# Kernel optimization log

Measured on AMD Instinct MI355X. Metric: run time of the kernel, lower is better.

## Reference

```python
import jax, jax.numpy as jnp
import numpy as np

B, S, ENC2, DEC = 32, 4096, 1024, 512

def setup_inputs() -> dict:
    key = jax.random.key(0)
    k1, k2, k3 = jax.random.split(key, 3)
    hidden = jax.random.normal(k1, (B, DEC), dtype=jnp.float32)
    context = jax.random.normal(k2, (B, S, ENC2), dtype=jnp.float32)
    mask = jnp.ones((B, S), dtype=jnp.int32)
    # Linear(enc*2+dec -> dec): weight [DEC, ENC2+DEC], bias [DEC]
    W_attn = jax.random.normal(k3, (DEC, ENC2 + DEC), dtype=jnp.float32) * (1.0 / np.sqrt(ENC2 + DEC))
    b_attn = jnp.zeros((DEC,), dtype=jnp.float32)
    v = jax.random.uniform(jax.random.fold_in(key, 7), (DEC,), dtype=jnp.float32)
    return {"hidden": hidden, "context": context, "mask": mask,
            "W_attn": W_attn, "b_attn": b_attn, "v": v}

def reference(hidden, context, mask, W_attn, b_attn, v):
    # cat((hidden repeated over S, context)) @ W.T == hidden@Wh.T + context@Wc.T
    # split W to avoid materializing the [B,S,1536] concat
    Wh = W_attn[:, :DEC]          # acts on hidden (first in cat)
    Wc = W_attn[:, DEC:]          # acts on context
    h_proj = hidden @ Wh.T + b_attn                      # [B, DEC]
    c_proj = jnp.einsum('bse,de->bsd', context, Wc)      # [B, S, DEC]
    sim = jnp.tanh(h_proj[:, None, :] + c_proj)          # [B, S, DEC]
    scores = jnp.einsum('bsd,d->bs', sim, v)             # [B, S]
    scores = jnp.where(mask == 0, -jnp.inf, scores)
    return jax.nn.softmax(scores, axis=1)
```

## Files before the change

kernel.cpp:

```cpp
#include <hip/hip_runtime.h>
#include <hip/hip_bf16.h>
#include <cmath>

#define NB 32
#define NS 4096
#define NK 1024
#define ND 512
#define WSTRIDE 1536
#define NTO 16

using bf16x8 = __attribute__((ext_vector_type(8))) __bf16;
using u16x8  = __attribute__((ext_vector_type(8))) unsigned short;
using f32x4  = __attribute__((ext_vector_type(4))) float;
typedef unsigned short u16;

__device__ inline u16 f2b(float x) {
    __hip_bfloat16 h = __float2bfloat16(x);
    u16 u; __builtin_memcpy(&u, &h, 2); return u;
}

__device__ inline float fast_tanh(float x) {
    float xc = fminf(fmaxf(x, -10.f), 10.f);
    float e = __expf(2.f * xc);
    return (e - 1.f) / (e + 1.f);
}

__global__ void pack_wc_kernel(const float* __restrict__ W, u16* __restrict__ wcb) {
    int idx = blockIdx.x * 256 + threadIdx.x;
    int R = idx >> 10, k = idx & 1023;
    float val = W[(size_t)R * WSTRIDE + ND + k];
    int ks = k >> 5, S = (k >> 3) & 3, j = k & 7;
    int g = ((R << 2) + S) ^ (R & 7);
    wcb[(ks << 14) + (g << 3) + j] = f2b(val);
}

__global__ void hproj_kernel(const float* __restrict__ hidden, const float* __restrict__ W,
                             const float* __restrict__ bias, float* __restrict__ hp) {
    int b = blockIdx.x, d = threadIdx.x;
    __shared__ float sh[ND];
    sh[d] = hidden[b * ND + d];
    __syncthreads();
    const float4* wr = (const float4*)(W + (size_t)d * WSTRIDE);
    float acc = bias[d];
#pragma unroll 8
    for (int k = 0; k < ND / 4; k++) {
        float4 w4 = wr[k];
        acc += w4.x * sh[4 * k] + w4.y * sh[4 * k + 1] + w4.z * sh[4 * k + 2] + w4.w * sh[4 * k + 3];
    }
    hp[b * ND + d] = acc;
}

__global__ __launch_bounds__(512, 1)
void fused_scores_kernel(const float* __restrict__ ctx, const u16* __restrict__ wcb,
                         const float* __restrict__ hp, const float* __restrict__ vvec,
                         float* __restrict__ scores) {
    __shared__ __align__(16) char lA[2][128 * 128];
    __shared__ __align__(16) char lB[2][512 * 64];
    __shared__ float shHp[ND];
    __shared__ float shV[ND];
    __shared__ float shSc[4][128];

    const int tid = threadIdx.x;
    const int blk = blockIdx.x;
    const int b  = blk >> 5;
    const int s0 = (blk & 31) << 7;

    shHp[tid] = hp[b * ND + tid];
    shV[tid]  = vvec[tid];

    const int lane = tid & 63, wid = tid >> 6;
    const int l15 = lane & 15, l4 = lane >> 4;
    const int wm = wid >> 2, wn = wid & 3;

    const int srow = tid >> 2, q = tid & 3;
    const float4* asrc = (const float4*)(ctx + (size_t)b * NS * NK + (size_t)(s0 + srow) * NK);
    const int awb0 = (srow << 7) + ((((q << 1) + 0) ^ (srow & 7)) << 4);
    const int awb1 = (srow << 7) + ((((q << 1) + 1) ^ (srow & 7)) << 4);

    int aoff[4], boff[8];
#pragma unroll
    for (int r = 0; r < 4; r++) {
        int row = (wm << 6) + (r << 4) + l15;
        aoff[r] = (row << 7) + ((l4 ^ (row & 7)) << 4);
    }
#pragma unroll
    for (int c = 0; c < 8; c++) {
        int row = (wn << 7) + (c << 4) + l15;
        boff[c] = ((row << 6) + (l4 << 4)) ^ ((row & 7) << 4);
    }

    f32x4 acc[4][8];
    f32x4 zero = {0.f, 0.f, 0.f, 0.f};
#pragma unroll
    for (int r = 0; r < 4; r++)
#pragma unroll
        for (int c = 0; c < 8; c++) acc[r][c] = zero;

    const char* wcb_bytes = (const char*)wcb;
    float4 va[4];

#define STAGE_B_DMA(chunk, buf)                                                      \
    _Pragma("unroll")                                                                \
    for (int i = 0; i < 4; i++) {                                                    \
        const char* src = wcb_bytes + ((size_t)(chunk) << 15)                        \
                          + (((((wid << 2) + i) << 6) + lane) << 4);                 \
        __builtin_amdgcn_global_load_lds(                                            \
            (const __attribute__((address_space(1))) void*)src,                      \
            (__attribute__((address_space(3))) void*)(&lB[buf][((wid << 2) + i) << 10]), \
            16, 0, 0);                                                               \
    }

#define LOAD_A_REGS(tile)                                                            \
    _Pragma("unroll")                                                                \
    for (int i = 0; i < 4; i++) va[i] = asrc[((tile) << 4) + (q << 2) + i];

#define CVT_WRITE_A(buf)                                                             \
    {                                                                                \
        u16x8 lo, hi;                                                                \
        lo[0] = f2b(va[0].x); lo[1] = f2b(va[0].y); lo[2] = f2b(va[0].z); lo[3] = f2b(va[0].w); \
        lo[4] = f2b(va[1].x); lo[5] = f2b(va[1].y); lo[6] = f2b(va[1].z); lo[7] = f2b(va[1].w); \
        hi[0] = f2b(va[2].x); hi[1] = f2b(va[2].y); hi[2] = f2b(va[2].z); hi[3] = f2b(va[2].w); \
        hi[4] = f2b(va[3].x); hi[5] = f2b(va[3].y); hi[6] = f2b(va[3].z); hi[7] = f2b(va[3].w); \
        *(u16x8*)(&lA[buf][awb0]) = lo;                                              \
        *(u16x8*)(&lA[buf][awb1]) = hi;                                              \
    }

#define MFMA_CLUSTER(abuf, axor, bbuf)                                               \
    {                                                                                \
        bf16x8 af[4], bfr[8];                                                        \
        _Pragma("unroll")                                                            \
        for (int r = 0; r < 4; r++) af[r] = *(const bf16x8*)(&lA[abuf][aoff[r] ^ (axor)]); \
        _Pragma("unroll")                                                            \
        for (int c = 0; c < 8; c++) bfr[c] = *(const bf16x8*)(&lB[bbuf][boff[c]]);   \
        __builtin_amdgcn_s_setprio(1);                                               \
        _Pragma("unroll")                                                            \
        for (int r = 0; r < 4; r++)                                                  \
            _Pragma("unroll")                                                        \
            for (int c = 0; c < 8; c++)                                              \
                acc[r][c] = __builtin_amdgcn_mfma_f32_16x16x32_bf16(af[r], bfr[c], acc[r][c], 0, 0, 0); \
        __builtin_amdgcn_s_setprio(0);                                               \
    }

    STAGE_B_DMA(0, 0);
    LOAD_A_REGS(0);
    asm volatile("s_waitcnt vmcnt(0)" ::: "memory");
    CVT_WRITE_A(0);
    LOAD_A_REGS(1);
    asm volatile("s_waitcnt lgkmcnt(0)" ::: "memory");
    __builtin_amdgcn_s_barrier();
    __builtin_amdgcn_sched_barrier(0);

#pragma unroll 2
    for (int t = 0; t < NTO; t++) {
        const int curA = t & 1, nxtA = curA ^ 1;
        const int u0 = t << 1;

        {
            const int cB = (u0 + 1 < 32) ? u0 + 1 : 31;
            STAGE_B_DMA(cB, 1);
            asm volatile("s_waitcnt vmcnt(4)" ::: "memory");
            CVT_WRITE_A(nxtA);
            const int tA = (t + 2 < NTO) ? t + 2 : NTO - 1;
            LOAD_A_REGS(tA);
            MFMA_CLUSTER(curA, 0, 0);
            asm volatile("s_waitcnt vmcnt(4) lgkmcnt(0)" ::: "memory");
            __builtin_amdgcn_s_barrier();
            __builtin_amdgcn_sched_barrier(0);
        }
        {
            const int cB = (u0 + 2 < 32) ? u0 + 2 : 31;
            STAGE_B_DMA(cB, 0);
            MFMA_CLUSTER(curA, 64, 1);
            asm volatile("s_waitcnt vmcnt(4) lgkmcnt(0)" ::: "memory");
            __builtin_amdgcn_s_barrier();
            __builtin_amdgcn_sched_barrier(0);
        }
    }

    float part[4][4];
#pragma unroll
    for (int r = 0; r < 4; r++)
#pragma unroll
        for (int i = 0; i < 4; i++) part[r][i] = 0.f;

#pragma unroll
    for (int r = 0; r < 4; r++) {
#pragma unroll
        for (int c = 0; c < 8; c++) {
            int d = (wn << 7) + (c << 4) + l15;
            float hpv = shHp[d], vv = shV[d];
#pragma unroll
            for (int i = 0; i < 4; i++) {
                float x = acc[r][c][i] + hpv;
                part[r][i] += fast_tanh(x) * vv;
            }
        }
    }

#pragma unroll
    for (int r = 0; r < 4; r++) {
#pragma unroll
        for (int i = 0; i < 4; i++) {
            float p = part[r][i];
            p += __shfl_xor(p, 1); p += __shfl_xor(p, 2);
            p += __shfl_xor(p, 4); p += __shfl_xor(p, 8);
            if (l15 == 0) shSc[wn][(wm << 6) + (r << 4) + (l4 << 2) + i] = p;
        }
    }
    __syncthreads();
    if (tid < 128) {
        float s = shSc[0][tid] + shSc[1][tid] + shSc[2][tid] + shSc[3][tid];
        scores[(size_t)b * NS + s0 + tid] = s;
    }
}

__global__ void softmax_kernel(const float* __restrict__ scores, const int* __restrict__ mask,
                               float* __restrict__ out) {
    int b = blockIdx.x, tid = threadIdx.x;
    __shared__ float red[256];
    float loc[16];
    float mx = -INFINITY;
#pragma unroll
    for (int i = 0; i < 16; i++) {
        int idx = i * 256 + tid;
        float s = scores[b * NS + idx];
        if (mask[b * NS + idx] == 0) s = -INFINITY;
        loc[i] = s;
        mx = fmaxf(mx, s);
    }
    red[tid] = mx; __syncthreads();
    for (int off = 128; off; off >>= 1) { if (tid < off) red[tid] = fmaxf(red[tid], red[tid + off]); __syncthreads(); }
    mx = red[0]; __syncthreads();
    float sum = 0.f;
#pragma unroll
    for (int i = 0; i < 16; i++) { float e = __expf(loc[i] - mx); loc[i] = e; sum += e; }
    red[tid] = sum; __syncthreads();
    for (int off = 128; off; off >>= 1) { if (tid < off) red[tid] += red[tid + off]; __syncthreads(); }
    float inv = 1.f / red[0];
#pragma unroll
    for (int i = 0; i < 16; i++) out[b * NS + i * 256 + tid] = loc[i] * inv;
}

extern "C" void kernel_launch(void* const* d_in, const int* in_sizes, int n_in,
                              void* d_out, int out_size, void* d_ws, size_t ws_size,
                              hipStream_t stream) {
    const float* hidden  = (const float*)d_in[0];
    const float* context = (const float*)d_in[1];
    const int*   mask    = (const int*)d_in[2];
    const float* W_attn  = (const float*)d_in[3];
    const float* b_attn  = (const float*)d_in[4];
    const float* v       = (const float*)d_in[5];
    float* out           = (float*)d_out;

    char* ws = (char*)d_ws;
    u16*   wcb    = (u16*)ws;
    float* hp     = (float*)(ws + (1 << 20));
    float* scores = (float*)(ws + (1 << 20) + (64 << 10));

    pack_wc_kernel<<<2048, 256, 0, stream>>>(W_attn, wcb);
    hproj_kernel<<<NB, ND, 0, stream>>>(hidden, W_attn, b_attn, hp);
    fused_scores_kernel<<<NB * 32, 512, 0, stream>>>(context, wcb, hp, v, scores);
    softmax_kernel<<<NB, 256, 0, stream>>>(scores, mask, out);
}
```

Measured before the change: 298.5 us.

## Halve M-tile to 64 rows and raise occupancy of fused scores kernel

Each block of the fused GEMM+tanh kernel now covers 64 sequence rows instead of 128, so the grid doubles. Accumulator registers and LDS shrink, and launch bounds allow up to 4 blocks per CU to improve latency hiding on the memory-bound context stream. The B-tile swizzle and its LDS read offsets are changed to a different bank-conflict pattern. Epilogue shared buffers are removed by reading hp/v straight from global memory and reusing lA for the reduction. As a trade-off, each W chunk is now loaded from L2 twice as often per context row, and the B DMA share per block grows relative to the compute it feeds.

After: 270.5 us. 9.4% less time.

```diff
diff --git a/kernel.cpp b/kernel.cpp
--- a/kernel.cpp
+++ b/kernel.cpp
@@ -30,7 +30,7 @@
     int R = idx >> 10, k = idx & 1023;
     float val = W[(size_t)R * WSTRIDE + ND + k];
     int ks = k >> 5, S = (k >> 3) & 3, j = k & 7;
-    int g = ((R << 2) + S) ^ (R & 7);
+    int g = (R << 2) + (S ^ ((R >> 1) & 3));
     wcb[(ks << 14) + (g << 3) + j] = f2b(val);
 }
 
@@ -50,54 +50,47 @@
     hp[b * ND + d] = acc;
 }
 
-__global__ __launch_bounds__(512, 1)
+__global__ __launch_bounds__(512, 4)
 void fused_scores_kernel(const float* __restrict__ ctx, const u16* __restrict__ wcb,
                          const float* __restrict__ hp, const float* __restrict__ vvec,
                          float* __restrict__ scores) {
-    __shared__ __align__(16) char lA[2][128 * 128];
+    __shared__ __align__(16) char lA[2][64 * 128];
     __shared__ __align__(16) char lB[2][512 * 64];
-    __shared__ float shHp[ND];
-    __shared__ float shV[ND];
-    __shared__ float shSc[4][128];
 
     const int tid = threadIdx.x;
     const int blk = blockIdx.x;
-    const int b  = blk >> 5;
-    const int s0 = (blk & 31) << 7;
-
-    shHp[tid] = hp[b * ND + tid];
-    shV[tid]  = vvec[tid];
+    const int b  = blk >> 6;
+    const int s0 = (blk & 63) << 6;
 
     const int lane = tid & 63, wid = tid >> 6;
     const int l15 = lane & 15, l4 = lane >> 4;
     const int wm = wid >> 2, wn = wid & 3;
 
-    const int srow = tid >> 2, q = tid & 3;
+    const int srow = tid >> 3, q = tid & 7;
     const float4* asrc = (const float4*)(ctx + (size_t)b * NS * NK + (size_t)(s0 + srow) * NK);
-    const int awb0 = (srow << 7) + ((((q << 1) + 0) ^ (srow & 7)) << 4);
-    const int awb1 = (srow << 7) + ((((q << 1) + 1) ^ (srow & 7)) << 4);
-
-    int aoff[4], boff[8];
-#pragma unroll
-    for (int r = 0; r < 4; r++) {
-        int row = (wm << 6) + (r << 4) + l15;
+    const int awbyte = (srow << 7) + ((q ^ (srow & 7)) << 4);
+
+    int aoff[2], boff[8];
+#pragma unroll
+    for (int r = 0; r < 2; r++) {
+        int row = (wm << 5) + (r << 4) + l15;
         aoff[r] = (row << 7) + ((l4 ^ (row & 7)) << 4);
     }
 #pragma unroll
     for (int c = 0; c < 8; c++) {
         int row = (wn << 7) + (c << 4) + l15;
-        boff[c] = ((row << 6) + (l4 << 4)) ^ ((row & 7) << 4);
-    }
-
-    f32x4 acc[4][8];
+        boff[c] = (row << 6) + ((l4 ^ ((row >> 1) & 3)) << 4);
+    }
+
+    f32x4 acc[2][8];
     f32x4 zero = {0.f, 0.f, 0.f, 0.f};
 #pragma unroll
-    for (int r = 0; r < 4; r++)
+    for (int r = 0; r < 2; r++)
 #pragma unroll
         for (int c = 0; c < 8; c++) acc[r][c] = zero;
 
     const char* wcb_bytes = (const char*)wcb;
-    float4 va[4];
+    float4 va0, va1;
 
 #define STAGE_B_DMA(chunk, buf)                                                      \
     _Pragma("unroll")                                                                \
@@ -111,34 +104,38 @@
     }
 
 #define LOAD_A_REGS(tile)                                                            \
-    _Pragma("unroll")                                                                \
-    for (int i = 0; i < 4; i++) va[i] = asrc[((tile) << 4) + (q << 2) + i];
+    {                                                                                \
+        va0 = asrc[((tile) << 4) + (q << 1)];                                        \
+        va1 = asrc[((tile) << 4) + (q << 1) + 1];                                    \
+    }
 
 #define CVT_WRITE_A(buf)                                                             \
     {                                                                                \
-        u16x8 lo, hi;                                                                \
-        lo[0] = f2b(va[0].x); lo[1] = f2b(va[0].y); lo[2] = f2b(va[0].z); lo[3] = f2b(va[0].w); \
-        lo[4] = f2b(va[1].x); lo[5] = f2b(va[1].y); lo[6] = f2b(va[1].z); lo[7] = f2b(va[1].w); \
-        hi[0] = f2b(va[2].x); hi[1] = f2b(va[2].y); hi[2] = f2b(va[2].z); hi[3] = f2b(va[2].w); \
-        hi[4] = f2b(va[3].x); hi[5] = f2b(va[3].y); hi[6] = f2b(va[3].z); hi[7] = f2b(va[3].w); \
-        *(u16x8*)(&lA[buf][awb0]) = lo;                                              \
-        *(u16x8*)(&lA[buf][awb1]) = hi;                                              \
+        u16x8 a8;                                                                    \
+        a8[0] = f2b(va0.x); a8[1] = f2b(va0.y); a8[2] = f2b(va0.z); a8[3] = f2b(va0.w); \
+        a8[4] = f2b(va1.x); a8[5] = f2b(va1.y); a8[6] = f2b(va1.z); a8[7] = f2b(va1.w); \
+        *(u16x8*)(&lA[buf][awbyte]) = a8;                                            \
     }
 
 #define MFMA_CLUSTER(abuf, axor, bbuf)                                               \
     {                                                                                \
-        bf16x8 af[4], bfr[8];                                                        \
+        bf16x8 af[2];                                                                \
         _Pragma("unroll")                                                            \
-        for (int r = 0; r < 4; r++) af[r] = *(const bf16x8*)(&lA[abuf][aoff[r] ^ (axor)]); \
+        for (int r = 0; r < 2; r++) af[r] = *(const bf16x8*)(&lA[abuf][aoff[r] ^ (axor)]); \
         _Pragma("unroll")                                                            \
-        for (int c = 0; c < 8; c++) bfr[c] = *(const bf16x8*)(&lB[bbuf][boff[c]]);   \
-        __builtin_amdgcn_s_setprio(1);                                               \
-        _Pragma("unroll")                                                            \
-        for (int r = 0; r < 4; r++)                                                  \
+        for (int ch = 0; ch < 2; ch++) {                                             \
+            bf16x8 bfr[4];                                                           \
             _Pragma("unroll")                                                        \
-            for (int c = 0; c < 8; c++)                                              \
-                acc[r][c] = __builtin_amdgcn_mfma_f32_16x16x32_bf16(af[r], bfr[c], acc[r][c], 0, 0, 0); \
-        __builtin_amdgcn_s_setprio(0);                                               \
+            for (int c = 0; c < 4; c++) bfr[c] = *(const bf16x8*)(&lB[bbuf][boff[ch * 4 + c]]); \
+            __builtin_amdgcn_s_setprio(1);                                           \
+            _Pragma("unroll")                                                        \
+            for (int r = 0; r < 2; r++)                                              \
+                _Pragma("unroll")                                                    \
+                for (int c = 0; c < 4; c++)                                          \
+                    acc[r][ch * 4 + c] = __builtin_amdgcn_mfma_f32_16x16x32_bf16(    \
+                        af[r], bfr[c], acc[r][ch * 4 + c], 0, 0, 0);                 \
+            __builtin_amdgcn_s_setprio(0);                                           \
+        }                                                                            \
     }
 
     STAGE_B_DMA(0, 0);
@@ -163,7 +160,7 @@
             const int tA = (t + 2 < NTO) ? t + 2 : NTO - 1;
             LOAD_A_REGS(tA);
             MFMA_CLUSTER(curA, 0, 0);
-            asm volatile("s_waitcnt vmcnt(4) lgkmcnt(0)" ::: "memory");
+            asm volatile("s_waitcnt vmcnt(2) lgkmcnt(0)" ::: "memory");
             __builtin_amdgcn_s_barrier();
             __builtin_amdgcn_sched_barrier(0);
         }
@@ -171,45 +168,44 @@
             const int cB = (u0 + 2 < 32) ? u0 + 2 : 31;
             STAGE_B_DMA(cB, 0);
             MFMA_CLUSTER(curA, 64, 1);
-            asm volatile("s_waitcnt vmcnt(4) lgkmcnt(0)" ::: "memory");
+            asm volatile("s_waitcnt lgkmcnt(0)" ::: "memory");
             __builtin_amdgcn_s_barrier();
             __builtin_amdgcn_sched_barrier(0);
         }
     }
 
-    float part[4][4];
-#pragma unroll
-    for (int r = 0; r < 4; r++)
+    const float* hpb = hp + b * ND;
+    float part[2][4];
+#pragma unroll
+    for (int r = 0; r < 2; r++)
 #pragma unroll
         for (int i = 0; i < 4; i++) part[r][i] = 0.f;
 
 #pragma unroll
-    for (int r = 0; r < 4; r++) {
-#pragma unroll
-        for (int c = 0; c < 8; c++) {
-            int d = (wn << 7) + (c << 4) + l15;
-            float hpv = shHp[d], vv = shV[d];
-#pragma unroll
-            for (int i = 0; i < 4; i++) {
-                float x = acc[r][c][i] + hpv;
-                part[r][i] += fast_tanh(x) * vv;
-            }
-        }
-    }
-
-#pragma unroll
-    for (int r = 0; r < 4; r++) {
+    for (int c = 0; c < 8; c++) {
+        int d = (wn << 7) + (c << 4) + l15;
+        float hpv = hpb[d], vv = vvec[d];
+#pragma unroll
+        for (int r = 0; r < 2; r++)
+#pragma unroll
+            for (int i = 0; i < 4; i++)
+                part[r][i] += fast_tanh(acc[r][c][i] + hpv) * vv;
+    }
+
+    float* sc = (float*)lA;
+#pragma unroll
+    for (int r = 0; r < 2; r++) {
 #pragma unroll
         for (int i = 0; i < 4; i++) {
             float p = part[r][i];
             p += __shfl_xor(p, 1); p += __shfl_xor(p, 2);
             p += __shfl_xor(p, 4); p += __shfl_xor(p, 8);
-            if (l15 == 0) shSc[wn][(wm << 6) + (r << 4) + (l4 << 2) + i] = p;
+            if (l15 == 0) sc[(wn << 6) + (wm << 5) + (r << 4) + (l4 << 2) + i] = p;
         }
     }
     __syncthreads();
-    if (tid < 128) {
-        float s = shSc[0][tid] + shSc[1][tid] + shSc[2][tid] + shSc[3][tid];
+    if (tid < 64) {
+        float s = sc[tid] + sc[64 + tid] + sc[128 + tid] + sc[192 + tid];
         scores[(size_t)b * NS + s0 + tid] = s;
     }
 }
@@ -259,6 +255,6 @@
 
     pack_wc_kernel<<<2048, 256, 0, stream>>>(W_attn, wcb);
     hproj_kernel<<<NB, ND, 0, stream>>>(hidden, W_attn, b_attn, hp);
-    fused_scores_kernel<<<NB * 32, 512, 0, stream>>>(context, wcb, hp, v, scores);
+    fused_scores_kernel<<<NB * 64, 512, 0, stream>>>(context, wcb, hp, v, scores);
     softmax_kernel<<<NB, 256, 0, stream>>>(scores, mask, out);
 }
```
